# Kernel tuning notes

Hardware: AMD Instinct MI355X
Metric: run time of the kernel (lower is better)

## Reference

```python
import jax, jax.numpy as jnp
import numpy as np

N_NODES = 100000
N_EDGES = 1_600_000
IN_DIM, HID, OUT_DIM, N_BLOCKS = 963, 192, 3, 6


def spmm(src, dst, w, x):
    # sparse adj @ x, adj[dst, src] = w  (COO edge list)
    msgs = x[src] * w[:, None]                      # [E, F]
    return jax.ops.segment_sum(msgs, dst, num_segments=N_NODES)


def gconv(x, src, dst, ew, w, lw, b):
    # Pixel2Mesh GConv: adj @ (x @ W) + x @ W_loop + b
    return spmm(src, dst, ew, x @ w) + x @ lw + b


def setup_inputs() -> dict:
    key = jax.random.key(0)
    ks = jax.random.split(key, 13)
    s = 0.02  # small init scale to keep deep stack numerically tame
    return {
        "inputs": jax.random.normal(ks[0], (N_NODES, IN_DIM), jnp.float32),
        "edge_src": jax.random.randint(ks[1], (N_EDGES,), 0, N_NODES),
        "edge_dst": jax.random.randint(ks[2], (N_EDGES,), 0, N_NODES),
        "edge_weight": jax.random.uniform(ks[3], (N_EDGES,), jnp.float32) / 16.0,
        "w_in": jax.random.normal(ks[4], (IN_DIM, HID), jnp.float32) * s,
        "loop_in": jax.random.normal(ks[5], (IN_DIM, HID), jnp.float32) * s,
        "b_in": jnp.zeros((HID,), jnp.float32),
        "blocks_w": jax.random.normal(ks[6], (N_BLOCKS, 2, HID, HID), jnp.float32) * s,
        "blocks_loop": jax.random.normal(ks[7], (N_BLOCKS, 2, HID, HID), jnp.float32) * s,
        "blocks_b": jnp.zeros((N_BLOCKS, 2, HID), jnp.float32),
        "w_out": jax.random.normal(ks[8], (HID, OUT_DIM), jnp.float32) * s,
        "loop_out": jax.random.normal(ks[9], (HID, OUT_DIM), jnp.float32) * s,
        "b_out": jnp.zeros((OUT_DIM,), jnp.float32),
    }


def reference(inputs, edge_src, edge_dst, edge_weight, w_in, loop_in, b_in,
              blocks_w, blocks_loop, blocks_b, w_out, loop_out, b_out):
    x = gconv(inputs, edge_src, edge_dst, edge_weight, w_in, loop_in, b_in)

    def block(x, params):
        bw, bl, bb = params
        h = gconv(x, edge_src, edge_dst, edge_weight, bw[0], bl[0], bb[0])
        h = gconv(h, edge_src, edge_dst, edge_weight, bw[1], bl[1], bb[1])
        return (x + h) * 0.5, None

    x_cat, _ = jax.lax.scan(block, x, (blocks_w, blocks_loop, blocks_b))
    x_out = gconv(x_cat, edge_src, edge_dst, edge_weight, w_out, loop_out, b_out)
    return (x_out, x_cat)
```

## Files before the change

### kernel.cpp

```cpp
#include <hip/hip_runtime.h>
#include <cstdint>
#include <cstddef>

#define N_NODES 100000
#define N_EDGES 1600000
#define IN_DIM 963
#define HID 192
#define OUT_DIM 3

typedef _Float16 f16x8 __attribute__((ext_vector_type(8)));
typedef float f32x4 __attribute__((ext_vector_type(4)));

__global__ void count_kernel(const int* __restrict__ dst, int* __restrict__ counts, int E) {
    int i = blockIdx.x * blockDim.x + threadIdx.x;
    if (i < E) atomicAdd(&counts[dst[i]], 1);
}

__global__ void scan_kernel(const int* __restrict__ counts, int* __restrict__ row_ptr, int n) {
    __shared__ int buf[1024];
    __shared__ int carry_s;
    int t = threadIdx.x;
    if (t == 0) { carry_s = 0; row_ptr[0] = 0; }
    __syncthreads();
    for (int base = 0; base < n; base += 1024) {
        int idx = base + t;
        int v = (idx < n) ? counts[idx] : 0;
        buf[t] = v;
        __syncthreads();
        for (int off = 1; off < 1024; off <<= 1) {
            int add = (t >= off) ? buf[t - off] : 0;
            __syncthreads();
            buf[t] += add;
            __syncthreads();
        }
        int carry = carry_s;
        if (idx < n) row_ptr[idx + 1] = carry + buf[t];
        __syncthreads();
        if (t == 1023) carry_s = carry + buf[1023];
        __syncthreads();
    }
}

__global__ void copy_cursor_kernel(const int* __restrict__ rp, int* __restrict__ cursor, int n) {
    int i = blockIdx.x * blockDim.x + threadIdx.x;
    if (i < n) cursor[i] = rp[i];
}

__global__ void scatter_kernel(const int* __restrict__ src, const int* __restrict__ dst,
                               const float* __restrict__ w, int* __restrict__ cursor,
                               int* __restrict__ csr_src, float* __restrict__ csr_w,
                               int* __restrict__ csr_eid, int E) {
    int i = blockIdx.x * blockDim.x + threadIdx.x;
    if (i < E) {
        int d = dst[i];
        int p = atomicAdd(&cursor[d], 1);
        csr_src[p] = src[i];
        csr_w[p] = w[i];
        csr_eid[p] = i;
    }
}

__global__ void sortrow_kernel(const int* __restrict__ rp, int* __restrict__ csr_src,
                               float* __restrict__ csr_w, int* __restrict__ csr_eid, int n) {
    int r = blockIdx.x * blockDim.x + threadIdx.x;
    if (r >= n) return;
    int s = rp[r], e = rp[r + 1];
    for (int i = s + 1; i < e; ++i) {
        int ke = csr_eid[i]; int ks = csr_src[i]; float kw = csr_w[i];
        int j = i - 1;
        while (j >= s && csr_eid[j] > ke) {
            csr_eid[j + 1] = csr_eid[j];
            csr_src[j + 1] = csr_src[j];
            csr_w[j + 1] = csr_w[j];
            --j;
        }
        csr_eid[j + 1] = ke; csr_src[j + 1] = ks; csr_w[j + 1] = kw;
    }
}

__global__ __launch_bounds__(256)
void trans_split(const float* __restrict__ W, const float* __restrict__ L,
                 int K, int Kp, _Float16* __restrict__ out_hi, _Float16* __restrict__ out_lo) {
    __shared__ float tile[32][33];
    const int n0 = blockIdx.x * 32, k0 = blockIdx.y * 32;
    const int tx = threadIdx.x, ty = threadIdx.y;
#pragma unroll
    for (int i = 0; i < 4; ++i) {
        int k = k0 + ty + i * 8;
        int n = n0 + tx;
        float v = 0.f;
        if (k < K) v = (n < HID) ? W[(size_t)k * HID + n] : L[(size_t)k * HID + (n - HID)];
        tile[ty + i * 8][tx] = v;
    }
    __syncthreads();
#pragma unroll
    for (int i = 0; i < 4; ++i) {
        int nl = ty + i * 8;
        int n = n0 + nl;
        int k = k0 + tx;
        float v = tile[tx][nl];
        _Float16 hi = (_Float16)v;
        _Float16 lo = (_Float16)(v - (float)hi);
        out_hi[(size_t)n * Kp + k] = hi;
        out_lo[(size_t)n * Kp + k] = lo;
    }
}

__global__ __launch_bounds__(256, 2)
void gemm_mfma(const float* __restrict__ X, int M, int Kx, int Kp,
               const _Float16* __restrict__ Wth, const _Float16* __restrict__ Wtl,
               const float* __restrict__ bias, const float* __restrict__ res,
               float* __restrict__ Hdst, float* __restrict__ Tdst) {
    __shared__ __align__(16) _Float16 Ah[2][4096];
    __shared__ __align__(16) _Float16 Al[2][4096];
    __shared__ __align__(16) _Float16 Bh[2][6144];
    __shared__ __align__(16) _Float16 Bl[2][6144];

    const int m0 = blockIdx.x * 128;
    const int bcol = blockIdx.y * 192;
    const int tid = threadIdx.x;
    const int lane = tid & 63;
    const int wave = tid >> 6;
    const int wr = wave >> 1;
    const int wc = wave & 1;

    const int ar = tid >> 1;
    const int ah_ = tid & 1;
    const int arow = m0 + ar;
    const bool arok = arow < M;
    const float* xrow = X + (size_t)(arok ? arow : 0) * Kx;

    float pa[16];
    f16x8 pbh[3], pbl[3];

    auto loadA = [&](int k0) {
        const int kb = k0 + ah_ * 16;
        if (arok && kb + 16 <= Kx) {
#pragma unroll
            for (int c = 0; c < 4; ++c) {
                f32x4 v = *(const f32x4*)(xrow + kb + c * 4);
#pragma unroll
                for (int j = 0; j < 4; ++j) pa[c * 4 + j] = v[j];
            }
        } else {
#pragma unroll
            for (int j = 0; j < 16; ++j)
                pa[j] = (arok && kb + j < Kx) ? xrow[kb + j] : 0.f;
        }
    };
    auto loadB = [&](int k0) {
#pragma unroll
        for (int c = 0; c < 3; ++c) {
            const int id = c * 256 + tid;
            const int idx = id >> 2, kg = id & 3;
            const size_t o = (size_t)(bcol + idx) * Kp + k0 + kg * 8;
            pbh[c] = *(const f16x8*)(Wth + o);
            pbl[c] = *(const f16x8*)(Wtl + o);
        }
    };
    auto stash = [&](int b) {
#pragma unroll
        for (int c = 0; c < 2; ++c) {
            const int kg = ah_ * 2 + c;
            f16x8 hi, lo;
#pragma unroll
            for (int j = 0; j < 8; ++j) {
                float x = pa[c * 8 + j];
                _Float16 h = (_Float16)x;
                hi[j] = h;
                lo[j] = (_Float16)(x - (float)h);
            }
            const int off = ar * 64 + ((kg ^ ar ^ (ar >> 2)) & 3) * 16;
            *(f16x8*)((char*)&Ah[b][0] + off) = hi;
            *(f16x8*)((char*)&Al[b][0] + off) = lo;
        }
#pragma unroll
        for (int c = 0; c < 3; ++c) {
            const int id = c * 256 + tid;
            const int idx = id >> 2, kg = id & 3;
            const int off = idx * 64 + ((kg ^ idx ^ (idx >> 2)) & 3) * 16;
            *(f16x8*)((char*)&Bh[b][0] + off) = pbh[c];
            *(f16x8*)((char*)&Bl[b][0] + off) = pbl[c];
        }
    };

    int a_off[4], b_off[6];
    const int kgl = lane >> 4;
#pragma unroll
    for (int mi = 0; mi < 4; ++mi) {
        const int idx = wr * 64 + mi * 16 + (lane & 15);
        a_off[mi] = idx * 64 + ((kgl ^ idx ^ (idx >> 2)) & 3) * 16;
    }
#pragma unroll
    for (int ni = 0; ni < 6; ++ni) {
        const int idx = wc * 96 + ni * 16 + (lane & 15);
        b_off[ni] = idx * 64 + ((kgl ^ idx ^ (idx >> 2)) & 3) * 16;
    }

    f32x4 acc[4][6];
#pragma unroll
    for (int i = 0; i < 4; ++i)
#pragma unroll
        for (int j = 0; j < 6; ++j)
            acc[i][j] = f32x4{0.f, 0.f, 0.f, 0.f};

    const int nsteps = (Kx + 31) / 32;
    loadA(0); loadB(0);

    for (int s = 0; s < nsteps; ++s) {
        const int b = s & 1;
        stash(b);
        if (s + 1 < nsteps) { loadA((s + 1) * 32); loadB((s + 1) * 32); }
        asm volatile("s_waitcnt lgkmcnt(0)" ::: "memory");
        __builtin_amdgcn_s_barrier();
        __builtin_amdgcn_sched_barrier(0);

        f16x8 fah[4], fal[4];
#pragma unroll
        for (int mi = 0; mi < 4; ++mi) {
            fah[mi] = *(const f16x8*)((char*)&Ah[b][0] + a_off[mi]);
            fal[mi] = *(const f16x8*)((char*)&Al[b][0] + a_off[mi]);
        }
#pragma unroll
        for (int ni = 0; ni < 6; ++ni) {
            const f16x8 fbh = *(const f16x8*)((char*)&Bh[b][0] + b_off[ni]);
            const f16x8 fbl = *(const f16x8*)((char*)&Bl[b][0] + b_off[ni]);
#pragma unroll
            for (int mi = 0; mi < 4; ++mi)
                acc[mi][ni] = __builtin_amdgcn_mfma_f32_16x16x32_f16(fah[mi], fbh, acc[mi][ni], 0, 0, 0);
#pragma unroll
            for (int mi = 0; mi < 4; ++mi)
                acc[mi][ni] = __builtin_amdgcn_mfma_f32_16x16x32_f16(fal[mi], fbh, acc[mi][ni], 0, 0, 0);
#pragma unroll
            for (int mi = 0; mi < 4; ++mi)
                acc[mi][ni] = __builtin_amdgcn_mfma_f32_16x16x32_f16(fah[mi], fbl, acc[mi][ni], 0, 0, 0);
        }
    }

    const bool isH = (bcol == 0);
#pragma unroll
    for (int mi = 0; mi < 4; ++mi) {
        const int rbase = m0 + wr * 64 + mi * 16 + ((lane >> 4) << 2);
#pragma unroll
        for (int ni = 0; ni < 6; ++ni) {
            const int gc = wc * 96 + ni * 16 + (lane & 15);
            f32x4 v = acc[mi][ni];
            if (isH) {
#pragma unroll
                for (int j = 0; j < 4; ++j) {
                    const int row = rbase + j;
                    if (row < M) Hdst[(size_t)row * HID + gc] = v[j];
                }
            } else {
                const float bv = bias[gc];
#pragma unroll
                for (int j = 0; j < 4; ++j) {
                    const int row = rbase + j;
                    if (row < M) {
                        float t = v[j] + bv;
                        if (res != nullptr) t += res[(size_t)row * HID + gc];
                        Tdst[(size_t)row * HID + gc] = t;
                    }
                }
            }
        }
    }
}

__global__ __launch_bounds__(256)
void spmm_kernel(const int* __restrict__ rp, const int* __restrict__ csrc,
                 const float* __restrict__ cw, const float* __restrict__ Hm,
                 float* __restrict__ out, float scale) {
    int wid = (blockIdx.x * 256 + threadIdx.x) >> 6;
    int lane = threadIdx.x & 63;
    if (wid >= N_NODES) return;
    int s = rp[wid], e = rp[wid + 1];
    float a0 = 0.f, a1 = 0.f, a2 = 0.f;
    int i = s;
    for (; i + 7 < e; i += 8) {
        float w[8];
        const float* h[8];
#pragma unroll
        for (int u = 0; u < 8; ++u) {
            w[u] = cw[i + u];
            h[u] = Hm + (size_t)csrc[i + u] * HID;
        }
#pragma unroll
        for (int u = 0; u < 8; ++u) {
            float x0 = h[u][lane], x1 = h[u][64 + lane], x2 = h[u][128 + lane];
            a0 += w[u] * x0; a1 += w[u] * x1; a2 += w[u] * x2;
        }
    }
    for (; i + 3 < e; i += 4) {
        float w[4];
        const float* h[4];
#pragma unroll
        for (int u = 0; u < 4; ++u) {
            w[u] = cw[i + u];
            h[u] = Hm + (size_t)csrc[i + u] * HID;
        }
#pragma unroll
        for (int u = 0; u < 4; ++u) {
            float x0 = h[u][lane], x1 = h[u][64 + lane], x2 = h[u][128 + lane];
            a0 += w[u] * x0; a1 += w[u] * x1; a2 += w[u] * x2;
        }
    }
    for (; i < e; ++i) {
        float w = cw[i];
        const float* h = Hm + (size_t)csrc[i] * HID;
        a0 += w * h[lane];
        a1 += w * h[64 + lane];
        a2 += w * h[128 + lane];
    }
    float* o = out + (size_t)wid * HID;
    o[lane]       = scale * (o[lane] + a0);
    o[64 + lane]  = scale * (o[64 + lane] + a1);
    o[128 + lane] = scale * (o[128 + lane] + a2);
}

__global__ __launch_bounds__(256)
void out_gemm(const float* __restrict__ X, const float* __restrict__ Wout,
              const float* __restrict__ Lout, const float* __restrict__ bout,
              float* __restrict__ H3, float* __restrict__ T3) {
    __shared__ float Ws[HID * OUT_DIM];
    __shared__ float Ls[HID * OUT_DIM];
    int tid = threadIdx.x;
    for (int i = tid; i < HID * OUT_DIM; i += 256) { Ws[i] = Wout[i]; Ls[i] = Lout[i]; }
    __syncthreads();
    int n = blockIdx.x * 4 + (tid >> 6);
    int lane = tid & 63;
    if (n >= N_NODES) return;
    const float* x = X + (size_t)n * HID;
    float aw[3] = {0.f, 0.f, 0.f}, al[3] = {0.f, 0.f, 0.f};
#pragma unroll
    for (int p = 0; p < 3; ++p) {
        int k = p * 64 + lane;
        float xv = x[k];
#pragma unroll
        for (int c = 0; c < 3; ++c) {
            aw[c] += xv * Ws[k * 3 + c];
            al[c] += xv * Ls[k * 3 + c];
        }
    }
#pragma unroll
    for (int off = 32; off > 0; off >>= 1) {
#pragma unroll
        for (int c = 0; c < 3; ++c) {
            aw[c] += __shfl_down(aw[c], off, 64);
            al[c] += __shfl_down(al[c], off, 64);
        }
    }
    if (lane == 0) {
#pragma unroll
        for (int c = 0; c < 3; ++c) {
            H3[n * 3 + c] = aw[c];
            T3[n * 3 + c] = al[c] + bout[c];
        }
    }
}

__global__ __launch_bounds__(256)
void out_spmm(const int* __restrict__ rp, const int* __restrict__ csrc,
              const float* __restrict__ cw, const float* __restrict__ H3,
              const float* __restrict__ T3, float* __restrict__ out) {
    int n = blockIdx.x * blockDim.x + threadIdx.x;
    if (n >= N_NODES) return;
    int s = rp[n], e = rp[n + 1];
    float a0 = 0.f, a1 = 0.f, a2 = 0.f;
    for (int i = s; i < e; ++i) {
        float w = cw[i];
        int src = csrc[i];
        a0 += w * H3[src * 3 + 0];
        a1 += w * H3[src * 3 + 1];
        a2 += w * H3[src * 3 + 2];
    }
    out[n * 3 + 0] = a0 + T3[n * 3 + 0];
    out[n * 3 + 1] = a1 + T3[n * 3 + 1];
    out[n * 3 + 2] = a2 + T3[n * 3 + 2];
}

extern "C" void kernel_launch(void* const* d_in, const int* in_sizes, int n_in,
                              void* d_out, int out_size, void* d_ws, size_t ws_size,
                              hipStream_t stream) {
    const float* X0    = (const float*)d_in[0];
    const int*   esrc  = (const int*)d_in[1];
    const int*   edst  = (const int*)d_in[2];
    const float* ew    = (const float*)d_in[3];
    const float* w_in  = (const float*)d_in[4];
    const float* l_in  = (const float*)d_in[5];
    const float* b_in  = (const float*)d_in[6];
    const float* bw    = (const float*)d_in[7];
    const float* bl    = (const float*)d_in[8];
    const float* bb    = (const float*)d_in[9];
    const float* w_out = (const float*)d_in[10];
    const float* l_out = (const float*)d_in[11];
    const float* b_out = (const float*)d_in[12];

    char* ws = (char*)d_ws;
    size_t off = 0;
    auto alloc = [&](size_t bytes) -> void* {
        void* p = ws + off;
        off += (bytes + 255) & ~(size_t)255;
        return p;
    };
    float* Hbuf   = (float*)alloc(sizeof(float) * (size_t)N_NODES * HID);
    float* h1     = (float*)alloc(sizeof(float) * (size_t)N_NODES * HID);
    int*   counts = (int*)alloc(sizeof(int) * N_NODES);
    int*   rp     = (int*)alloc(sizeof(int) * (N_NODES + 1));
    int*   cursor = (int*)alloc(sizeof(int) * N_NODES);
    int*   csrc   = (int*)alloc(sizeof(int) * N_EDGES);
    float* cw     = (float*)alloc(sizeof(float) * N_EDGES);
    int*   ceid   = (int*)alloc(sizeof(int) * N_EDGES);
    float* H3     = (float*)alloc(sizeof(float) * (size_t)N_NODES * OUT_DIM);
    float* T3     = (float*)alloc(sizeof(float) * (size_t)N_NODES * OUT_DIM);
    const int KP0 = 992;
    _Float16* Wt0h = (_Float16*)alloc(sizeof(_Float16) * 384 * KP0);
    _Float16* Wt0l = (_Float16*)alloc(sizeof(_Float16) * 384 * KP0);
    _Float16* WtHh = (_Float16*)alloc(sizeof(_Float16) * 12 * 384 * HID);
    _Float16* WtHl = (_Float16*)alloc(sizeof(_Float16) * 12 * 384 * HID);

    float* xout = (float*)d_out;
    float* xcat = (float*)d_out + (size_t)N_NODES * OUT_DIM;

    trans_split<<<dim3(12, 31), dim3(32, 8), 0, stream>>>(w_in, l_in, IN_DIM, KP0, Wt0h, Wt0l);
    for (int l = 0; l < 12; ++l) {
        trans_split<<<dim3(12, 6), dim3(32, 8), 0, stream>>>(
            bw + (size_t)l * HID * HID, bl + (size_t)l * HID * HID, HID, HID,
            WtHh + (size_t)l * 384 * HID, WtHl + (size_t)l * 384 * HID);
    }

    hipMemsetAsync(counts, 0, sizeof(int) * N_NODES, stream);
    count_kernel<<<(N_EDGES + 255) / 256, 256, 0, stream>>>(edst, counts, N_EDGES);
    scan_kernel<<<1, 1024, 0, stream>>>(counts, rp, N_NODES);
    copy_cursor_kernel<<<(N_NODES + 255) / 256, 256, 0, stream>>>(rp, cursor, N_NODES);
    scatter_kernel<<<(N_EDGES + 255) / 256, 256, 0, stream>>>(esrc, edst, ew, cursor,
                                                              csrc, cw, ceid, N_EDGES);
    sortrow_kernel<<<(N_NODES + 255) / 256, 256, 0, stream>>>(rp, csrc, cw, ceid, N_NODES);

    const dim3 gemm_grid((N_NODES + 127) / 128, 2);
    const int spmm_blocks = (N_NODES * 64 + 255) / 256;

    gemm_mfma<<<gemm_grid, 256, 0, stream>>>(X0, N_NODES, IN_DIM, KP0, Wt0h, Wt0l,
                                             b_in, nullptr, Hbuf, xcat);
    spmm_kernel<<<spmm_blocks, 256, 0, stream>>>(rp, csrc, cw, Hbuf, xcat, 1.0f);

    for (int b = 0; b < 6; ++b) {
        int l0 = b * 2, l1 = b * 2 + 1;
        const float* B0 = bb + (size_t)l0 * HID;
        const float* B1 = bb + (size_t)l1 * HID;

        gemm_mfma<<<gemm_grid, 256, 0, stream>>>(xcat, N_NODES, HID, HID,
                                                 WtHh + (size_t)l0 * 384 * HID,
                                                 WtHl + (size_t)l0 * 384 * HID,
                                                 B0, nullptr, Hbuf, h1);
        spmm_kernel<<<spmm_blocks, 256, 0, stream>>>(rp, csrc, cw, Hbuf, h1, 1.0f);
        gemm_mfma<<<gemm_grid, 256, 0, stream>>>(h1, N_NODES, HID, HID,
                                                 WtHh + (size_t)l1 * 384 * HID,
                                                 WtHl + (size_t)l1 * 384 * HID,
                                                 B1, xcat, Hbuf, xcat);
        spmm_kernel<<<spmm_blocks, 256, 0, stream>>>(rp, csrc, cw, Hbuf, xcat, 0.5f);
    }

    out_gemm<<<(N_NODES + 3) / 4, 256, 0, stream>>>(xcat, w_out, l_out, b_out, H3, T3);
    out_spmm<<<(N_NODES + 255) / 256, 256, 0, stream>>>(rp, csrc, cw, H3, T3, xout);
}
```

Baseline: 4.651 ms.

## Stage GEMM tiles via direct global-to-LDS loads and split fp16 at fragment read

Replaces the register-staged GEMM with one that uses global_load_lds to copy raw fp32 activation tiles and fp16 weight tiles straight into a double-buffered, XOR-swizzled LDS region. The hi/lo fp16 split of A now happens after the fragment is read from LDS, not before the LDS store. This is meant to remove register staging and the conversion work on the load path, and to overlap the next tile's fetch with the MFMA work. In exchange it doubles the A tile's LDS footprint, with 80KB per block, and repeats the A conversion in both column waves. For K=963 it also reads past the row end without zero-fill and relies on the weight padding being zero.

```diff
diff --git a/kernel.cpp b/kernel.cpp
--- a/kernel.cpp
+++ b/kernel.cpp
@@ -107,95 +107,50 @@
 }
 
 __global__ __launch_bounds__(256, 2)
-void gemm_mfma(const float* __restrict__ X, int M, int Kx, int Kp,
-               const _Float16* __restrict__ Wth, const _Float16* __restrict__ Wtl,
-               const float* __restrict__ bias, const float* __restrict__ res,
-               float* __restrict__ Hdst, float* __restrict__ Tdst) {
-    __shared__ __align__(16) _Float16 Ah[2][4096];
-    __shared__ __align__(16) _Float16 Al[2][4096];
-    __shared__ __align__(16) _Float16 Bh[2][6144];
-    __shared__ __align__(16) _Float16 Bl[2][6144];
+void gemm_lds(const float* __restrict__ X, int M, int Kx, int Kp,
+              const _Float16* __restrict__ Wth, const _Float16* __restrict__ Wtl,
+              const float* __restrict__ bias, const float* __restrict__ res,
+              float* __restrict__ Hdst, float* __restrict__ Tdst) {
+    __shared__ __align__(16) char smem[81920];
 
     const int m0 = blockIdx.x * 128;
-    const int bcol = blockIdx.y * 192;
     const int tid = threadIdx.x;
     const int lane = tid & 63;
     const int wave = tid >> 6;
     const int wr = wave >> 1;
     const int wc = wave & 1;
-
-    const int ar = tid >> 1;
-    const int ah_ = tid & 1;
-    const int arow = m0 + ar;
-    const bool arok = arow < M;
-    const float* xrow = X + (size_t)(arok ? arow : 0) * Kx;
-
-    float pa[16];
-    f16x8 pbh[3], pbl[3];
-
-    auto loadA = [&](int k0) {
-        const int kb = k0 + ah_ * 16;
-        if (arok && kb + 16 <= Kx) {
-#pragma unroll
-            for (int c = 0; c < 4; ++c) {
-                f32x4 v = *(const f32x4*)(xrow + kb + c * 4);
-#pragma unroll
-                for (int j = 0; j < 4; ++j) pa[c * 4 + j] = v[j];
-            }
-        } else {
-#pragma unroll
-            for (int j = 0; j < 16; ++j)
-                pa[j] = (arok && kb + j < Kx) ? xrow[kb + j] : 0.f;
+    const int kg = lane >> 4;
+    const int bcol = blockIdx.y * 192;
+
+    auto stage = [&](int k0, int cb) {
+#pragma unroll
+        for (int i = 0; i < 4; ++i) {
+            const int id = i * 256 + tid;
+            const int row = id >> 3, slot = id & 7;
+            int gr = m0 + row; if (gr >= M) gr = 0;
+            const int srck = k0 + ((slot ^ (row & 7)) << 2);
+            const float* src = X + (size_t)gr * Kx + srck;
+            void* dst = (void*)(smem + cb + (i * 256 + wave * 64) * 16);
+            __builtin_amdgcn_global_load_lds(
+                (const __attribute__((address_space(1))) void*)src,
+                (__attribute__((address_space(3))) void*)dst, 16, 0, 0);
+        }
+#pragma unroll
+        for (int i = 0; i < 3; ++i) {
+            const int id = i * 256 + tid;
+            const int row = id >> 2, slot = id & 3;
+            const int srck = k0 + ((slot ^ ((row >> 1) & 3)) << 3);
+            const size_t go = (size_t)(bcol + row) * Kp + srck;
+            void* dsth = (void*)(smem + cb + 16384 + (i * 256 + wave * 64) * 16);
+            void* dstl = (void*)(smem + cb + 28672 + (i * 256 + wave * 64) * 16);
+            __builtin_amdgcn_global_load_lds(
+                (const __attribute__((address_space(1))) void*)(Wth + go),
+                (__attribute__((address_space(3))) void*)dsth, 16, 0, 0);
+            __builtin_amdgcn_global_load_lds(
+                (const __attribute__((address_space(1))) void*)(Wtl + go),
+                (__attribute__((address_space(3))) void*)dstl, 16, 0, 0);
         }
     };
-    auto loadB = [&](int k0) {
-#pragma unroll
-        for (int c = 0; c < 3; ++c) {
-            const int id = c * 256 + tid;
-            const int idx = id >> 2, kg = id & 3;
-            const size_t o = (size_t)(bcol + idx) * Kp + k0 + kg * 8;
-            pbh[c] = *(const f16x8*)(Wth + o);
-            pbl[c] = *(const f16x8*)(Wtl + o);
-        }
-    };
-    auto stash = [&](int b) {
-#pragma unroll
-        for (int c = 0; c < 2; ++c) {
-            const int kg = ah_ * 2 + c;
-            f16x8 hi, lo;
-#pragma unroll
-            for (int j = 0; j < 8; ++j) {
-                float x = pa[c * 8 + j];
-                _Float16 h = (_Float16)x;
-                hi[j] = h;
-                lo[j] = (_Float16)(x - (float)h);
-            }
-            const int off = ar * 64 + ((kg ^ ar ^ (ar >> 2)) & 3) * 16;
-            *(f16x8*)((char*)&Ah[b][0] + off) = hi;
-            *(f16x8*)((char*)&Al[b][0] + off) = lo;
-        }
-#pragma unroll
-        for (int c = 0; c < 3; ++c) {
-            const int id = c * 256 + tid;
-            const int idx = id >> 2, kg = id & 3;
-            const int off = idx * 64 + ((kg ^ idx ^ (idx >> 2)) & 3) * 16;
-            *(f16x8*)((char*)&Bh[b][0] + off) = pbh[c];
-            *(f16x8*)((char*)&Bl[b][0] + off) = pbl[c];
-        }
-    };
-
-    int a_off[4], b_off[6];
-    const int kgl = lane >> 4;
-#pragma unroll
-    for (int mi = 0; mi < 4; ++mi) {
-        const int idx = wr * 64 + mi * 16 + (lane & 15);
-        a_off[mi] = idx * 64 + ((kgl ^ idx ^ (idx >> 2)) & 3) * 16;
-    }
-#pragma unroll
-    for (int ni = 0; ni < 6; ++ni) {
-        const int idx = wc * 96 + ni * 16 + (lane & 15);
-        b_off[ni] = idx * 64 + ((kgl ^ idx ^ (idx >> 2)) & 3) * 16;
-    }
 
     f32x4 acc[4][6];
 #pragma unroll
@@ -205,26 +160,39 @@
             acc[i][j] = f32x4{0.f, 0.f, 0.f, 0.f};
 
     const int nsteps = (Kx + 31) / 32;
-    loadA(0); loadB(0);
+
+    stage(0, 0);
+    __syncthreads();
 
     for (int s = 0; s < nsteps; ++s) {
-        const int b = s & 1;
-        stash(b);
-        if (s + 1 < nsteps) { loadA((s + 1) * 32); loadB((s + 1) * 32); }
-        asm volatile("s_waitcnt lgkmcnt(0)" ::: "memory");
-        __builtin_amdgcn_s_barrier();
-        __builtin_amdgcn_sched_barrier(0);
-
+        const int cb = (s & 1) * 40960;
+        if (s + 1 < nsteps) stage((s + 1) * 32, ((s + 1) & 1) * 40960);
+
+        const char* cur = smem + cb;
         f16x8 fah[4], fal[4];
 #pragma unroll
         for (int mi = 0; mi < 4; ++mi) {
-            fah[mi] = *(const f16x8*)((char*)&Ah[b][0] + a_off[mi]);
-            fal[mi] = *(const f16x8*)((char*)&Al[b][0] + a_off[mi]);
+            const int row = wr * 64 + mi * 16 + (lane & 15);
+            const char* rb = cur + row * 128;
+            f32x4 a0 = *(const f32x4*)(rb + ((((2 * kg)     ^ (row & 7))) << 4));
+            f32x4 a1 = *(const f32x4*)(rb + ((((2 * kg + 1) ^ (row & 7))) << 4));
+            f16x8 hi, lo;
+#pragma unroll
+            for (int j = 0; j < 4; ++j) {
+                float x0 = a0[j], x1 = a1[j];
+                _Float16 h0 = (_Float16)x0, h1 = (_Float16)x1;
+                hi[j] = h0;     hi[4 + j] = h1;
+                lo[j] = (_Float16)(x0 - (float)h0);
+                lo[4 + j] = (_Float16)(x1 - (float)h1);
+            }
+            fah[mi] = hi; fal[mi] = lo;
         }
 #pragma unroll
         for (int ni = 0; ni < 6; ++ni) {
-            const f16x8 fbh = *(const f16x8*)((char*)&Bh[b][0] + b_off[ni]);
-            const f16x8 fbl = *(const f16x8*)((char*)&Bl[b][0] + b_off[ni]);
+            const int idx = wc * 96 + ni * 16 + (lane & 15);
+            const int off = 16384 + idx * 64 + ((kg ^ ((idx >> 1) & 3)) << 4);
+            const f16x8 fbh = *(const f16x8*)(cur + off);
+            const f16x8 fbl = *(const f16x8*)(cur + off + 12288);
 #pragma unroll
             for (int mi = 0; mi < 4; ++mi)
                 acc[mi][ni] = __builtin_amdgcn_mfma_f32_16x16x32_f16(fah[mi], fbh, acc[mi][ni], 0, 0, 0);
@@ -235,6 +203,7 @@
             for (int mi = 0; mi < 4; ++mi)
                 acc[mi][ni] = __builtin_amdgcn_mfma_f32_16x16x32_f16(fah[mi], fbl, acc[mi][ni], 0, 0, 0);
         }
+        __syncthreads();
     }
 
     const bool isH = (bcol == 0);
@@ -440,8 +409,8 @@
     const dim3 gemm_grid((N_NODES + 127) / 128, 2);
     const int spmm_blocks = (N_NODES * 64 + 255) / 256;
 
-    gemm_mfma<<<gemm_grid, 256, 0, stream>>>(X0, N_NODES, IN_DIM, KP0, Wt0h, Wt0l,
-                                             b_in, nullptr, Hbuf, xcat);
+    gemm_lds<<<gemm_grid, 256, 0, stream>>>(X0, N_NODES, IN_DIM, KP0, Wt0h, Wt0l,
+                                            b_in, nullptr, Hbuf, xcat);
     spmm_kernel<<<spmm_blocks, 256, 0, stream>>>(rp, csrc, cw, Hbuf, xcat, 1.0f);
 
     for (int b = 0; b < 6; ++b) {
@@ -449,15 +418,15 @@
         const float* B0 = bb + (size_t)l0 * HID;
         const float* B1 = bb + (size_t)l1 * HID;
 
-        gemm_mfma<<<gemm_grid, 256, 0, stream>>>(xcat, N_NODES, HID, HID,
-                                                 WtHh + (size_t)l0 * 384 * HID,
-                                                 WtHl + (size_t)l0 * 384 * HID,
-                                                 B0, nullptr, Hbuf, h1);
+        gemm_lds<<<gemm_grid, 256, 0, stream>>>(xcat, N_NODES, HID, HID,
+                                                WtHh + (size_t)l0 * 384 * HID,
+                                                WtHl + (size_t)l0 * 384 * HID,
+                                                B0, nullptr, Hbuf, h1);
         spmm_kernel<<<spmm_blocks, 256, 0, stream>>>(rp, csrc, cw, Hbuf, h1, 1.0f);
-        gemm_mfma<<<gemm_grid, 256, 0, stream>>>(h1, N_NODES, HID, HID,
-                                                 WtHh + (size_t)l1 * 384 * HID,
-                                                 WtHl + (size_t)l1 * 384 * HID,
-                                                 B1, xcat, Hbuf, xcat);
+        gemm_lds<<<gemm_grid, 256, 0, stream>>>(h1, N_NODES, HID, HID,
+                                                WtHh + (size_t)l1 * 384 * HID,
+                                                WtHl + (size_t)l1 * 384 * HID,
+                                                B1, xcat, Hbuf, xcat);
         spmm_kernel<<<spmm_blocks, 256, 0, stream>>>(rp, csrc, cw, Hbuf, xcat, 0.5f);
     }
 
```

New measurement: 4.646 ms. About the same (-0.1%).
